# Kernel tuning notes

Measured on AMD Instinct MI355X. Metric: run time of the kernel, lower is better.

The kernel has to match this reference:

```python
import jax, jax.numpy as jnp
import numpy as np

DIM = 1024
SEQ = 4096
HEADS = 16
DH = 64
KPROJ = 64
MLP = 4096
EPS = 1e-5


def layer_norm(x, g, b):
    mu = jnp.mean(x, axis=-1, keepdims=True)
    var = jnp.mean(jnp.square(x - mu), axis=-1, keepdims=True)
    return (x - mu) * jax.lax.rsqrt(var + EPS) * g + b


def setup_inputs() -> dict:
    key = jax.random.key(0)
    ks = jax.random.split(key, 12)
    s = 0.02
    return {
        "x": jax.random.normal(ks[0], (4, SEQ, DIM), jnp.float32),
        "Wq": jax.random.normal(ks[1], (DIM, HEADS * DH), jnp.float32) * s,
        "Wk": jax.random.normal(ks[2], (DIM, HEADS * DH), jnp.float32) * s,
        "Wv": jax.random.normal(ks[3], (DIM, HEADS * DH), jnp.float32) * s,
        "E": jax.random.normal(ks[4], (SEQ, KPROJ), jnp.float32),
        "Fm": jax.random.normal(ks[5], (SEQ, KPROJ), jnp.float32),
        "Wo": jax.random.normal(ks[6], (HEADS * DH, DIM), jnp.float32) * s,
        "bo": jnp.zeros((DIM,), jnp.float32),
        "ln1_g": jnp.ones((DIM,), jnp.float32),
        "ln1_b": jnp.zeros((DIM,), jnp.float32),
        "ln2_g": jnp.ones((DIM,), jnp.float32),
        "ln2_b": jnp.zeros((DIM,), jnp.float32),
        "W1": jax.random.normal(ks[7], (DIM, MLP), jnp.float32) * s,
        "b1": jnp.zeros((MLP,), jnp.float32),
        "W2": jax.random.normal(ks[8], (MLP, DIM), jnp.float32) * s,
        "b2": jnp.zeros((DIM,), jnp.float32),
    }


def reference(x, Wq, Wk, Wv, E, Fm, Wo, bo, ln1_g, ln1_b, ln2_g, ln2_b, W1, b1, W2, b2):
    B, S, D = x.shape
    scale = DH ** -0.5
    # --- Linformer attention (pre-norm) ---
    xn = layer_norm(x, ln1_g, ln1_b)
    q = (xn @ Wq).reshape(B, S, HEADS, DH).transpose(0, 2, 1, 3)  # b h s d
    k = (xn @ Wk).reshape(B, S, HEADS, DH).transpose(0, 2, 1, 3)
    v = (xn @ Wv).reshape(B, S, HEADS, DH).transpose(0, 2, 1, 3)
    # Faithful to source: i and n are summed independently (rank-1 projection)
    kE = jnp.einsum('bhid,nk->bhkd', k, E)   # b h k d
    vF = jnp.einsum('bhid,nk->bhkd', v, Fm)  # b h k d
    dots = jnp.einsum('bhsd,bhkd->bhsk', q, kE) * scale
    attn = jax.nn.softmax(dots, axis=-1)
    out = jnp.einsum('bhsk,bhkd->bhsd', attn, vF)
    out = out.transpose(0, 2, 1, 3).reshape(B, S, HEADS * DH)
    x = x + out @ Wo + bo
    # --- MLP (pre-norm) ---
    xn2 = layer_norm(x, ln2_g, ln2_b)
    h = jax.nn.gelu(xn2 @ W1 + b1, approximate=False)
    x = x + h @ W2 + b2
    return x
```

## Files before the change

kernel.cpp:

```cpp
#include <hip/hip_runtime.h>
#include <hip/hip_bf16.h>

#define DIMD 1024
#define SEQL 4096
#define BATCH 4
#define NHEADS 16
#define DHEAD 64
#define KPROJ 64
#define MLPD 4096
#define NTOK (BATCH*SEQL)
#define EPSV 1e-5f

using short8 = __attribute__((ext_vector_type(8))) short;
using f32x4  = __attribute__((ext_vector_type(4))) float;

__device__ __forceinline__ float wave_reduce_sum(float v) {
    #pragma unroll
    for (int off = 32; off > 0; off >>= 1) v += __shfl_down(v, off, 64);
    return v;
}

__global__ __launch_bounds__(256) void k_stats1(const float* __restrict__ x,
                                                float* __restrict__ stats) {
    int t = blockIdx.x;
    const float4 x4 = *(const float4*)(x + (size_t)t*DIMD + threadIdx.x*4);
    float s  = x4.x + x4.y + x4.z + x4.w;
    float ss = x4.x*x4.x + x4.y*x4.y + x4.z*x4.z + x4.w*x4.w;
    s = wave_reduce_sum(s); ss = wave_reduce_sum(ss);
    __shared__ float rs[4], rss[4];
    int wave = threadIdx.x >> 6, lane = threadIdx.x & 63;
    if (lane == 0) { rs[wave] = s; rss[wave] = ss; }
    __syncthreads();
    if (threadIdx.x == 0) {
        float S1 = rs[0]+rs[1]+rs[2]+rs[3];
        float S2 = rss[0]+rss[1]+rss[2]+rss[3];
        float mu = S1 * (1.0f/DIMD);
        float var = S2 * (1.0f/DIMD) - mu*mu;
        stats[2*t]   = mu;
        stats[2*t+1] = rsqrtf(var + EPSV);
    }
}

__global__ __launch_bounds__(256) void k_xnsum(const float* __restrict__ x,
                                               const float* __restrict__ stats,
                                               const float* __restrict__ g1,
                                               const float* __restrict__ be1,
                                               float* __restrict__ xnsum) {
    int b = blockIdx.x >> 6, sc = blockIdx.x & 63;
    int d = threadIdx.x * 4;
    int t0 = b*SEQL + sc*64;
    float a0=0,a1=0,a2=0,a3=0;
    for (int s = 0; s < 64; s++) {
        int t = t0 + s;
        float mu = stats[2*t], rstd = stats[2*t+1];
        const float4 x4 = *(const float4*)(x + (size_t)t*DIMD + d);
        a0 += (x4.x-mu)*rstd; a1 += (x4.y-mu)*rstd;
        a2 += (x4.z-mu)*rstd; a3 += (x4.w-mu)*rstd;
    }
    const float4 g4 = *(const float4*)(g1 + d);
    const float4 b4 = *(const float4*)(be1 + d);
    atomicAdd(&xnsum[b*DIMD + d + 0], a0*g4.x + 64.0f*b4.x);
    atomicAdd(&xnsum[b*DIMD + d + 1], a1*g4.y + 64.0f*b4.y);
    atomicAdd(&xnsum[b*DIMD + d + 2], a2*g4.z + 64.0f*b4.z);
    atomicAdd(&xnsum[b*DIMD + d + 3], a3*g4.w + 64.0f*b4.w);
}

__global__ __launch_bounds__(256) void k_efsum(const float* __restrict__ E,
                                               const float* __restrict__ Fm,
                                               float* __restrict__ Esum,
                                               float* __restrict__ Fsum) {
    int g = blockIdx.x;
    int k = threadIdx.x & 63, seg = threadIdx.x >> 6;
    __shared__ float red[4][64];
    int n0 = g*256 + seg*64;
    float pe = 0, pf = 0;
    for (int i = 0; i < 64; i++) {
        pe += E [(size_t)(n0+i)*KPROJ + k];
        pf += Fm[(size_t)(n0+i)*KPROJ + k];
    }
    red[seg][k] = pe; __syncthreads();
    if (seg == 0) atomicAdd(&Esum[k], red[0][k]+red[1][k]+red[2][k]+red[3][k]);
    __syncthreads();
    red[seg][k] = pf; __syncthreads();
    if (seg == 0) atomicAdd(&Fsum[k], red[0][k]+red[1][k]+red[2][k]+red[3][k]);
}

__global__ __launch_bounds__(256) void k_kvsum(const float* __restrict__ xnsum,
                                               const float* __restrict__ Wk,
                                               const float* __restrict__ Wv,
                                               float* __restrict__ Ksum,
                                               float* __restrict__ Vsum) {
    int i = blockIdx.x;
    int b = i >> 3, which = (i >> 2) & 1, jc = i & 3;
    const float* W = which ? Wv : Wk;
    float* outp = which ? Vsum : Ksum;
    int j = jc*256 + threadIdx.x;
    __shared__ float xs[DIMD];
    for (int d = threadIdx.x; d < DIMD; d += 256) xs[d] = xnsum[b*DIMD + d];
    __syncthreads();
    float acc = 0;
    #pragma unroll 8
    for (int d = 0; d < DIMD; d++) acc += xs[d] * W[(size_t)d*DIMD + j];
    outp[b*DIMD + j] = acc;
}

__global__ __launch_bounds__(256) void k_mt(const float* __restrict__ Wq,
                                            const float* __restrict__ Ksum,
                                            float* __restrict__ Mt) {
    int i = blockIdx.x;
    int dc = i & 3, h = (i >> 2) & 15, b = i >> 6;
    __shared__ float ks[DHEAD];
    if (threadIdx.x < DHEAD) ks[threadIdx.x] = Ksum[b*DIMD + h*DHEAD + threadIdx.x];
    __syncthreads();
    int d = dc*256 + threadIdx.x;
    float acc = 0;
    #pragma unroll 8
    for (int j = 0; j < DHEAD; j++) acc += Wq[(size_t)d*DIMD + h*DHEAD + j] * ks[j];
    Mt[((size_t)b*NHEADS + h)*DIMD + d] = acc;
}

__global__ __launch_bounds__(256) void k_p(const float* __restrict__ Wo,
                                           const float* __restrict__ Vsum,
                                           float* __restrict__ P) {
    int i = blockIdx.x;
    int dc = i & 3, h = (i >> 2) & 15, b = i >> 6;
    __shared__ float vs[DHEAD];
    if (threadIdx.x < DHEAD) vs[threadIdx.x] = Vsum[b*DIMD + h*DHEAD + threadIdx.x];
    __syncthreads();
    int d = dc*256 + threadIdx.x;
    float acc = 0;
    #pragma unroll 8
    for (int j = 0; j < DHEAD; j++) acc += vs[j] * Wo[(size_t)(h*DHEAD + j)*DIMD + d];
    P[((size_t)b*NHEADS + h)*DIMD + d] = acc;
}

__global__ __launch_bounds__(256) void k_attn_apply(
    const float* __restrict__ x, const float* __restrict__ stats,
    const float* __restrict__ Mt, const float* __restrict__ P,
    const float* __restrict__ Esum, const float* __restrict__ Fsum,
    const float* __restrict__ g1, const float* __restrict__ be1,
    const float* __restrict__ bo,
    const float* __restrict__ g2, const float* __restrict__ be2,
    float* __restrict__ y, __hip_bfloat16* __restrict__ xn2) {
    __shared__ float xn_s[DIMD];
    __shared__ float qk_s[NHEADS];
    __shared__ float w_s[NHEADS];
    __shared__ float red2[8];
    __shared__ float mu2_s, rs2_s;
    int t = blockIdx.x;
    int b = t >> 12;
    int tid = threadIdx.x;
    int wave = tid >> 6, lane = tid & 63;
    float mu = stats[2*t], rstd = stats[2*t+1];
    int d4 = tid * 4;
    const float4 x4  = *(const float4*)(x + (size_t)t*DIMD + d4);
    const float4 g14 = *(const float4*)(g1 + d4);
    const float4 b14 = *(const float4*)(be1 + d4);
    float xnv0 = (x4.x-mu)*rstd*g14.x + b14.x;
    float xnv1 = (x4.y-mu)*rstd*g14.y + b14.y;
    float xnv2 = (x4.z-mu)*rstd*g14.z + b14.z;
    float xnv3 = (x4.w-mu)*rstd*g14.w + b14.w;
    xn_s[d4+0]=xnv0; xn_s[d4+1]=xnv1; xn_s[d4+2]=xnv2; xn_s[d4+3]=xnv3;
    __syncthreads();
    for (int hh = 0; hh < 4; hh++) {
        int h = wave*4 + hh;
        const float* Mh = Mt + ((size_t)b*NHEADS + h)*DIMD;
        float p = 0;
        #pragma unroll
        for (int i = 0; i < 16; i++) { int d = lane + i*64; p += xn_s[d]*Mh[d]; }
        p = wave_reduce_sum(p);
        if (lane == 0) qk_s[h] = p;
    }
    __syncthreads();
    const float scale = 0.125f;
    float ek = Esum[lane], fk = Fsum[lane];
    for (int hh = 0; hh < 4; hh++) {
        int h = wave*4 + hh;
        float c = qk_s[h] * scale;
        float logit = c * ek;
        float m = logit;
        #pragma unroll
        for (int off = 32; off > 0; off >>= 1) m = fmaxf(m, __shfl_down(m, off, 64));
        m = __shfl(m, 0, 64);
        float e = expf(logit - m);
        float s1 = e, s2 = e * fk;
        #pragma unroll
        for (int off = 32; off > 0; off >>= 1) {
            s1 += __shfl_down(s1, off, 64);
            s2 += __shfl_down(s2, off, 64);
        }
        if (lane == 0) w_s[h] = s2 / s1;
    }
    __syncthreads();
    const float4 bo4 = *(const float4*)(bo + d4);
    float y0 = x4.x + bo4.x, y1 = x4.y + bo4.y, y2 = x4.z + bo4.z, y3 = x4.w + bo4.w;
    #pragma unroll
    for (int h = 0; h < NHEADS; h++) {
        float wv = w_s[h];
        const float4 p4 = *(const float4*)(P + ((size_t)b*NHEADS + h)*DIMD + d4);
        y0 += wv*p4.x; y1 += wv*p4.y; y2 += wv*p4.z; y3 += wv*p4.w;
    }
    float4 yo; yo.x = y0; yo.y = y1; yo.z = y2; yo.w = y3;
    *(float4*)(y + (size_t)t*DIMD + d4) = yo;
    float s  = y0+y1+y2+y3;
    float ss = y0*y0+y1*y1+y2*y2+y3*y3;
    s = wave_reduce_sum(s); ss = wave_reduce_sum(ss);
    if (lane == 0) { red2[wave] = s; red2[4+wave] = ss; }
    __syncthreads();
    if (tid == 0) {
        float S1 = red2[0]+red2[1]+red2[2]+red2[3];
        float S2 = red2[4]+red2[5]+red2[6]+red2[7];
        float m2 = S1*(1.0f/DIMD);
        float v2 = S2*(1.0f/DIMD) - m2*m2;
        mu2_s = m2; rs2_s = rsqrtf(v2 + EPSV);
    }
    __syncthreads();
    float mu2 = mu2_s, rs2 = rs2_s;
    const float4 g24 = *(const float4*)(g2 + d4);
    const float4 b24 = *(const float4*)(be2 + d4);
    union { __hip_bfloat16 h4[4]; uint2 v; } pk;
    pk.h4[0] = __float2bfloat16((y0-mu2)*rs2*g24.x + b24.x);
    pk.h4[1] = __float2bfloat16((y1-mu2)*rs2*g24.y + b24.y);
    pk.h4[2] = __float2bfloat16((y2-mu2)*rs2*g24.z + b24.z);
    pk.h4[3] = __float2bfloat16((y3-mu2)*rs2*g24.w + b24.w);
    *(uint2*)((char*)(xn2 + (size_t)t*DIMD + d4)) = pk.v;
}

__global__ __launch_bounds__(256) void k_transpose_bf16(const float* __restrict__ src,
                                                        __hip_bfloat16* __restrict__ dst,
                                                        int R, int C) {
    __shared__ float tile[32][33];
    int c0 = blockIdx.x * 32, r0 = blockIdx.y * 32;
    int tx = threadIdx.x & 31, ty = threadIdx.x >> 5;
    #pragma unroll
    for (int i = 0; i < 32; i += 8)
        tile[ty+i][tx] = src[(size_t)(r0+ty+i)*C + c0 + tx];
    __syncthreads();
    #pragma unroll
    for (int i = 0; i < 32; i += 8)
        dst[(size_t)(c0+ty+i)*R + r0 + tx] = __float2bfloat16(tile[tx][ty+i]);
}

template <int EPI>
__global__ __launch_bounds__(256) void k_gemm_bt(
    const __hip_bfloat16* __restrict__ A, const __hip_bfloat16* __restrict__ Bt,
    const float* __restrict__ bias, void* __restrict__ Cout,
    int M, int N, int K) {
    __shared__ __align__(16) unsigned short As[128*32];
    __shared__ __align__(16) unsigned short Bs[128*32];
    const int m0 = blockIdx.x * 128, n0 = blockIdx.y * 128;
    const int tid = threadIdx.x;
    const int wave = tid >> 6, lane = tid & 63;
    const int wm = (wave & 1) * 64, wn = (wave >> 1) * 64;
    const int quad = lane >> 4, l15 = lane & 15;
    f32x4 acc[4][4];
    #pragma unroll
    for (int i = 0; i < 4; i++)
        #pragma unroll
        for (int j = 0; j < 4; j++) acc[i][j] = 0;
    const int srow = tid >> 2, scol = (tid & 3) * 8;
    const unsigned short* Au = (const unsigned short*)A;
    const unsigned short* Bu = (const unsigned short*)Bt;
    for (int k0 = 0; k0 < K; k0 += 32) {
        uint4 a0 = *(const uint4*)(Au + (size_t)(m0+srow   )*K + k0 + scol);
        uint4 a1 = *(const uint4*)(Au + (size_t)(m0+srow+64)*K + k0 + scol);
        uint4 b0 = *(const uint4*)(Bu + (size_t)(n0+srow   )*K + k0 + scol);
        uint4 b1 = *(const uint4*)(Bu + (size_t)(n0+srow+64)*K + k0 + scol);
        __syncthreads();
        *(uint4*)&As[srow*32 + scol]      = a0;
        *(uint4*)&As[(srow+64)*32 + scol] = a1;
        *(uint4*)&Bs[srow*32 + scol]      = b0;
        *(uint4*)&Bs[(srow+64)*32 + scol] = b1;
        __syncthreads();
        short8 af[4], bf[4];
        #pragma unroll
        for (int mt = 0; mt < 4; mt++)
            af[mt] = *(const short8*)&As[(wm + mt*16 + l15)*32 + quad*8];
        #pragma unroll
        for (int nt = 0; nt < 4; nt++)
            bf[nt] = *(const short8*)&Bs[(wn + nt*16 + l15)*32 + quad*8];
        #pragma unroll
        for (int mt = 0; mt < 4; mt++)
            #pragma unroll
            for (int nt = 0; nt < 4; nt++)
                acc[mt][nt] = __builtin_amdgcn_mfma_f32_16x16x32_bf16(af[mt], bf[nt], acc[mt][nt], 0, 0, 0);
    }
    #pragma unroll
    for (int nt = 0; nt < 4; nt++) {
        int col = n0 + wn + nt*16 + l15;
        float bv = bias[col];
        #pragma unroll
        for (int mt = 0; mt < 4; mt++) {
            #pragma unroll
            for (int r = 0; r < 4; r++) {
                int row = m0 + wm + mt*16 + quad*4 + r;
                float v = acc[mt][nt][r] + bv;
                if (EPI == 0) {
                    float gl = 0.5f * v * (1.0f + erff(v * 0.70710678118654752f));
                    ((__hip_bfloat16*)Cout)[(size_t)row*N + col] = __float2bfloat16(gl);
                } else {
                    ((float*)Cout)[(size_t)row*N + col] += v;
                }
            }
        }
    }
}

extern "C" void kernel_launch(void* const* d_in, const int* in_sizes, int n_in,
                              void* d_out, int out_size, void* d_ws, size_t ws_size,
                              hipStream_t stream) {
    const float* x   = (const float*)d_in[0];
    const float* Wq  = (const float*)d_in[1];
    const float* Wk  = (const float*)d_in[2];
    const float* Wv  = (const float*)d_in[3];
    const float* E   = (const float*)d_in[4];
    const float* Fm  = (const float*)d_in[5];
    const float* Wo  = (const float*)d_in[6];
    const float* bo  = (const float*)d_in[7];
    const float* g1  = (const float*)d_in[8];
    const float* be1 = (const float*)d_in[9];
    const float* g2  = (const float*)d_in[10];
    const float* be2 = (const float*)d_in[11];
    const float* W1  = (const float*)d_in[12];
    const float* bb1 = (const float*)d_in[13];
    const float* W2  = (const float*)d_in[14];
    const float* bb2 = (const float*)d_in[15];
    float* outp = (float*)d_out;

    char* ws = (char*)d_ws;
    size_t o = 0;
    auto alloc = [&](size_t bytes) -> char* {
        char* r = ws + o;
        o = (o + bytes + 255) & ~(size_t)255;
        return r;
    };
    float* xnsum = (float*)alloc((size_t)BATCH*DIMD*4);
    float* Esum  = (float*)alloc(KPROJ*4);
    float* Fsum  = (float*)alloc(KPROJ*4);
    float* stats = (float*)alloc((size_t)NTOK*2*4);
    float* Ksum  = (float*)alloc((size_t)BATCH*DIMD*4);
    float* Vsum  = (float*)alloc((size_t)BATCH*DIMD*4);
    float* Mt    = (float*)alloc((size_t)BATCH*NHEADS*DIMD*4);
    float* P     = (float*)alloc((size_t)BATCH*NHEADS*DIMD*4);
    __hip_bfloat16* xn2  = (__hip_bfloat16*)alloc((size_t)NTOK*DIMD*2);
    __hip_bfloat16* W1T  = (__hip_bfloat16*)alloc((size_t)DIMD*MLPD*2);
    __hip_bfloat16* W2T  = (__hip_bfloat16*)alloc((size_t)MLPD*DIMD*2);
    __hip_bfloat16* hbuf = (__hip_bfloat16*)alloc((size_t)NTOK*MLPD*2);

    hipMemsetAsync(xnsum, 0, (size_t)BATCH*DIMD*4, stream);
    hipMemsetAsync(Esum, 0, KPROJ*4, stream);
    hipMemsetAsync(Fsum, 0, KPROJ*4, stream);

    k_stats1<<<dim3(NTOK), dim3(256), 0, stream>>>(x, stats);
    k_xnsum<<<dim3(BATCH*64), dim3(256), 0, stream>>>(x, stats, g1, be1, xnsum);
    k_efsum<<<dim3(16), dim3(256), 0, stream>>>(E, Fm, Esum, Fsum);
    k_kvsum<<<dim3(32), dim3(256), 0, stream>>>(xnsum, Wk, Wv, Ksum, Vsum);
    k_mt<<<dim3(256), dim3(256), 0, stream>>>(Wq, Ksum, Mt);
    k_p<<<dim3(256), dim3(256), 0, stream>>>(Wo, Vsum, P);
    k_attn_apply<<<dim3(NTOK), dim3(256), 0, stream>>>(
        x, stats, Mt, P, Esum, Fsum, g1, be1, bo, g2, be2, outp, xn2);
    k_transpose_bf16<<<dim3(MLPD/32, DIMD/32), dim3(256), 0, stream>>>(W1, W1T, DIMD, MLPD);
    k_transpose_bf16<<<dim3(DIMD/32, MLPD/32), dim3(256), 0, stream>>>(W2, W2T, MLPD, DIMD);
    k_gemm_bt<0><<<dim3(NTOK/128, MLPD/128), dim3(256), 0, stream>>>(
        xn2, W1T, bb1, (void*)hbuf, NTOK, MLPD, DIMD);
    k_gemm_bt<1><<<dim3(NTOK/128, DIMD/128), dim3(256), 0, stream>>>(
        hbuf, W2T, bb2, (void*)outp, NTOK, DIMD, MLPD);
}
```

Baseline: 884.7 us.

## Batch tokens per block in attn_apply and use direct global-to-LDS loads in GEMM

k_attn_apply now handles 8 tokens per block, so the per-head Mt and P rows are loaded once and reused across tokens, and the synchronisations are shared across tokens. The GEMM tile loads switch from register-staged global loads plus LDS stores to the global_load_lds builtin, which writes 16 bytes straight into shared memory. This is meant to cut VGPR pressure and instruction count in the MFMA GEMMs. The GEMM still has no double buffering, so the async copies do not overlap with compute, and the per-lane 16-byte LDS write layout must match the fragment reads for results to stay correct.

After: 967.1 us. 9.3% more time.

```diff
diff --git a/kernel.cpp b/kernel.cpp
--- a/kernel.cpp
+++ b/kernel.cpp
@@ -10,6 +10,7 @@
 #define MLPD 4096
 #define NTOK (BATCH*SEQL)
 #define EPSV 1e-5f
+#define TPB 8
 
 using short8 = __attribute__((ext_vector_type(8))) short;
 using f32x4  = __attribute__((ext_vector_type(4))) float;
@@ -18,6 +19,13 @@
     #pragma unroll
     for (int off = 32; off > 0; off >>= 1) v += __shfl_down(v, off, 64);
     return v;
+}
+
+__device__ __forceinline__ void async_cp16(const unsigned short* g, unsigned short* l) {
+    __builtin_amdgcn_global_load_lds(
+        (const __attribute__((address_space(1))) unsigned int*)g,
+        (__attribute__((address_space(3))) unsigned int*)l,
+        16, 0, 0);
 }
 
 __global__ __launch_bounds__(256) void k_stats1(const float* __restrict__ x,
@@ -142,88 +150,104 @@
     const float* __restrict__ bo,
     const float* __restrict__ g2, const float* __restrict__ be2,
     float* __restrict__ y, __hip_bfloat16* __restrict__ xn2) {
-    __shared__ float xn_s[DIMD];
-    __shared__ float qk_s[NHEADS];
-    __shared__ float w_s[NHEADS];
-    __shared__ float red2[8];
-    __shared__ float mu2_s, rs2_s;
-    int t = blockIdx.x;
-    int b = t >> 12;
-    int tid = threadIdx.x;
-    int wave = tid >> 6, lane = tid & 63;
-    float mu = stats[2*t], rstd = stats[2*t+1];
-    int d4 = tid * 4;
-    const float4 x4  = *(const float4*)(x + (size_t)t*DIMD + d4);
+    __shared__ float red[TPB][NHEADS][4];
+    __shared__ float w_s[TPB][NHEADS];
+    __shared__ float red2[TPB][8];
+    __shared__ float st2[TPB][2];
+    const int t0 = blockIdx.x * TPB;
+    const int b = t0 >> 12;
+    const int tid = threadIdx.x;
+    const int wave = tid >> 6, lane = tid & 63;
+    const int d4 = tid * 4;
+
     const float4 g14 = *(const float4*)(g1 + d4);
     const float4 b14 = *(const float4*)(be1 + d4);
-    float xnv0 = (x4.x-mu)*rstd*g14.x + b14.x;
-    float xnv1 = (x4.y-mu)*rstd*g14.y + b14.y;
-    float xnv2 = (x4.z-mu)*rstd*g14.z + b14.z;
-    float xnv3 = (x4.w-mu)*rstd*g14.w + b14.w;
-    xn_s[d4+0]=xnv0; xn_s[d4+1]=xnv1; xn_s[d4+2]=xnv2; xn_s[d4+3]=xnv3;
-    __syncthreads();
-    for (int hh = 0; hh < 4; hh++) {
-        int h = wave*4 + hh;
-        const float* Mh = Mt + ((size_t)b*NHEADS + h)*DIMD;
-        float p = 0;
-        #pragma unroll
-        for (int i = 0; i < 16; i++) { int d = lane + i*64; p += xn_s[d]*Mh[d]; }
-        p = wave_reduce_sum(p);
-        if (lane == 0) qk_s[h] = p;
-    }
-    __syncthreads();
-    const float scale = 0.125f;
-    float ek = Esum[lane], fk = Fsum[lane];
-    for (int hh = 0; hh < 4; hh++) {
-        int h = wave*4 + hh;
-        float c = qk_s[h] * scale;
-        float logit = c * ek;
-        float m = logit;
-        #pragma unroll
-        for (int off = 32; off > 0; off >>= 1) m = fmaxf(m, __shfl_down(m, off, 64));
-        m = __shfl(m, 0, 64);
-        float e = expf(logit - m);
-        float s1 = e, s2 = e * fk;
-        #pragma unroll
-        for (int off = 32; off > 0; off >>= 1) {
-            s1 += __shfl_down(s1, off, 64);
-            s2 += __shfl_down(s2, off, 64);
+    float4 xf[TPB], xn[TPB];
+    #pragma unroll
+    for (int t = 0; t < TPB; t++) {
+        xf[t] = *(const float4*)(x + (size_t)(t0+t)*DIMD + d4);
+        float mu = stats[2*(t0+t)], rstd = stats[2*(t0+t)+1];
+        xn[t].x = (xf[t].x-mu)*rstd*g14.x + b14.x;
+        xn[t].y = (xf[t].y-mu)*rstd*g14.y + b14.y;
+        xn[t].z = (xf[t].z-mu)*rstd*g14.z + b14.z;
+        xn[t].w = (xf[t].w-mu)*rstd*g14.w + b14.w;
+    }
+    #pragma unroll
+    for (int h = 0; h < NHEADS; h++) {
+        const float4 m4 = *(const float4*)(Mt + ((size_t)b*NHEADS + h)*DIMD + d4);
+        #pragma unroll
+        for (int t = 0; t < TPB; t++) {
+            float p = xn[t].x*m4.x + xn[t].y*m4.y + xn[t].z*m4.z + xn[t].w*m4.w;
+            p = wave_reduce_sum(p);
+            if (lane == 0) red[t][h][wave] = p;
         }
-        if (lane == 0) w_s[h] = s2 / s1;
+    }
+    __syncthreads();
+    {
+        const float scale = 0.125f;
+        const float ek = Esum[lane], fk = Fsum[lane];
+        for (int pi = wave; pi < TPB*NHEADS; pi += 4) {
+            int t = pi >> 4, h = pi & 15;
+            float qk = red[t][h][0]+red[t][h][1]+red[t][h][2]+red[t][h][3];
+            float logit = qk * scale * ek;
+            float m = logit;
+            #pragma unroll
+            for (int off = 32; off > 0; off >>= 1) m = fmaxf(m, __shfl_down(m, off, 64));
+            m = __shfl(m, 0, 64);
+            float e = expf(logit - m);
+            float s1 = e, s2 = e * fk;
+            #pragma unroll
+            for (int off = 32; off > 0; off >>= 1) {
+                s1 += __shfl_down(s1, off, 64);
+                s2 += __shfl_down(s2, off, 64);
+            }
+            if (lane == 0) w_s[t][h] = s2 / s1;
+        }
     }
     __syncthreads();
     const float4 bo4 = *(const float4*)(bo + d4);
-    float y0 = x4.x + bo4.x, y1 = x4.y + bo4.y, y2 = x4.z + bo4.z, y3 = x4.w + bo4.w;
-    #pragma unroll
-    for (int h = 0; h < NHEADS; h++) {
-        float wv = w_s[h];
-        const float4 p4 = *(const float4*)(P + ((size_t)b*NHEADS + h)*DIMD + d4);
-        y0 += wv*p4.x; y1 += wv*p4.y; y2 += wv*p4.z; y3 += wv*p4.w;
-    }
-    float4 yo; yo.x = y0; yo.y = y1; yo.z = y2; yo.w = y3;
-    *(float4*)(y + (size_t)t*DIMD + d4) = yo;
-    float s  = y0+y1+y2+y3;
-    float ss = y0*y0+y1*y1+y2*y2+y3*y3;
-    s = wave_reduce_sum(s); ss = wave_reduce_sum(ss);
-    if (lane == 0) { red2[wave] = s; red2[4+wave] = ss; }
-    __syncthreads();
-    if (tid == 0) {
-        float S1 = red2[0]+red2[1]+red2[2]+red2[3];
-        float S2 = red2[4]+red2[5]+red2[6]+red2[7];
+    float4 p4[NHEADS];
+    #pragma unroll
+    for (int h = 0; h < NHEADS; h++)
+        p4[h] = *(const float4*)(P + ((size_t)b*NHEADS + h)*DIMD + d4);
+    #pragma unroll
+    for (int t = 0; t < TPB; t++) {
+        float y0 = xf[t].x + bo4.x, y1 = xf[t].y + bo4.y;
+        float y2 = xf[t].z + bo4.z, y3 = xf[t].w + bo4.w;
+        #pragma unroll
+        for (int h = 0; h < NHEADS; h++) {
+            float wv = w_s[t][h];
+            y0 += wv*p4[h].x; y1 += wv*p4[h].y; y2 += wv*p4[h].z; y3 += wv*p4[h].w;
+        }
+        float4 yo; yo.x = y0; yo.y = y1; yo.z = y2; yo.w = y3;
+        *(float4*)(y + (size_t)(t0+t)*DIMD + d4) = yo;
+        xf[t] = yo;
+        float s  = y0+y1+y2+y3;
+        float ss = y0*y0+y1*y1+y2*y2+y3*y3;
+        s = wave_reduce_sum(s); ss = wave_reduce_sum(ss);
+        if (lane == 0) { red2[t][wave] = s; red2[t][4+wave] = ss; }
+    }
+    __syncthreads();
+    if (tid < TPB) {
+        float S1 = red2[tid][0]+red2[tid][1]+red2[tid][2]+red2[tid][3];
+        float S2 = red2[tid][4]+red2[tid][5]+red2[tid][6]+red2[tid][7];
         float m2 = S1*(1.0f/DIMD);
         float v2 = S2*(1.0f/DIMD) - m2*m2;
-        mu2_s = m2; rs2_s = rsqrtf(v2 + EPSV);
-    }
-    __syncthreads();
-    float mu2 = mu2_s, rs2 = rs2_s;
+        st2[tid][0] = m2; st2[tid][1] = rsqrtf(v2 + EPSV);
+    }
+    __syncthreads();
     const float4 g24 = *(const float4*)(g2 + d4);
     const float4 b24 = *(const float4*)(be2 + d4);
-    union { __hip_bfloat16 h4[4]; uint2 v; } pk;
-    pk.h4[0] = __float2bfloat16((y0-mu2)*rs2*g24.x + b24.x);
-    pk.h4[1] = __float2bfloat16((y1-mu2)*rs2*g24.y + b24.y);
-    pk.h4[2] = __float2bfloat16((y2-mu2)*rs2*g24.z + b24.z);
-    pk.h4[3] = __float2bfloat16((y3-mu2)*rs2*g24.w + b24.w);
-    *(uint2*)((char*)(xn2 + (size_t)t*DIMD + d4)) = pk.v;
+    #pragma unroll
+    for (int t = 0; t < TPB; t++) {
+        float mu2 = st2[t][0], rs2 = st2[t][1];
+        union { __hip_bfloat16 h4[4]; uint2 v; } pk;
+        pk.h4[0] = __float2bfloat16((xf[t].x-mu2)*rs2*g24.x + b24.x);
+        pk.h4[1] = __float2bfloat16((xf[t].y-mu2)*rs2*g24.y + b24.y);
+        pk.h4[2] = __float2bfloat16((xf[t].z-mu2)*rs2*g24.z + b24.z);
+        pk.h4[3] = __float2bfloat16((xf[t].w-mu2)*rs2*g24.w + b24.w);
+        *(uint2*)((char*)(xn2 + (size_t)(t0+t)*DIMD + d4)) = pk.v;
+    }
 }
 
 __global__ __launch_bounds__(256) void k_transpose_bf16(const float* __restrict__ src,
@@ -258,19 +282,23 @@
     for (int i = 0; i < 4; i++)
         #pragma unroll
         for (int j = 0; j < 4; j++) acc[i][j] = 0;
-    const int srow = tid >> 2, scol = (tid & 3) * 8;
+
     const unsigned short* Au = (const unsigned short*)A;
     const unsigned short* Bu = (const unsigned short*)Bt;
+    const int srow = (wave*2)*16 + (lane >> 2);
+    const int scol = (lane & 3) * 8;
+    const unsigned short* Ag = Au + (size_t)(m0 + srow)*K + scol;
+    const unsigned short* Bg = Bu + (size_t)(n0 + srow)*K + scol;
+    unsigned short* Al = As + (wave*2)*512;
+    unsigned short* Bl = Bs + (wave*2)*512;
+
     for (int k0 = 0; k0 < K; k0 += 32) {
-        uint4 a0 = *(const uint4*)(Au + (size_t)(m0+srow   )*K + k0 + scol);
-        uint4 a1 = *(const uint4*)(Au + (size_t)(m0+srow+64)*K + k0 + scol);
-        uint4 b0 = *(const uint4*)(Bu + (size_t)(n0+srow   )*K + k0 + scol);
-        uint4 b1 = *(const uint4*)(Bu + (size_t)(n0+srow+64)*K + k0 + scol);
         __syncthreads();
-        *(uint4*)&As[srow*32 + scol]      = a0;
-        *(uint4*)&As[(srow+64)*32 + scol] = a1;
-        *(uint4*)&Bs[srow*32 + scol]      = b0;
-        *(uint4*)&Bs[(srow+64)*32 + scol] = b1;
+        async_cp16(Ag,          Al);
+        async_cp16(Ag + 16*(size_t)K, Al + 512);
+        async_cp16(Bg,          Bl);
+        async_cp16(Bg + 16*(size_t)K, Bl + 512);
+        Ag += 32; Bg += 32;
         __syncthreads();
         short8 af[4], bf[4];
         #pragma unroll
@@ -357,7 +385,7 @@
     k_kvsum<<<dim3(32), dim3(256), 0, stream>>>(xnsum, Wk, Wv, Ksum, Vsum);
     k_mt<<<dim3(256), dim3(256), 0, stream>>>(Wq, Ksum, Mt);
     k_p<<<dim3(256), dim3(256), 0, stream>>>(Wo, Vsum, P);
-    k_attn_apply<<<dim3(NTOK), dim3(256), 0, stream>>>(
+    k_attn_apply<<<dim3(NTOK/TPB), dim3(256), 0, stream>>>(
         x, stats, Mt, P, Esum, Fsum, g1, be1, bo, g2, be2, outp, xn2);
     k_transpose_bf16<<<dim3(MLPD/32, DIMD/32), dim3(256), 0, stream>>>(W1, W1T, DIMD, MLPD);
     k_transpose_bf16<<<dim3(DIMD/32, MLPD/32), dim3(256), 0, stream>>>(W2, W2T, MLPD, DIMD);
```
